# Kernel tuning notes

Hardware: AMD Instinct MI355X
Metric: run time of the kernel (lower is better)

The kernel has to match this reference:

```python
import jax, jax.numpy as jnp
import numpy as np

N = 50000
HEADS = 8
NEG_SLOPE = 0.2


def gat_layer(x, W, a_src, a_dst, b, src, dst, heads, n):
    # x: [N, Fin], W: [Fin, heads*C], a_src/a_dst: [heads, C], b: [heads*C]
    C = W.shape[1] // heads
    h = (x @ W).reshape(n, heads, C)                      # [N, H, C]
    al_s = jnp.einsum('nhc,hc->nh', h, a_src)             # [N, H]
    al_d = jnp.einsum('nhc,hc->nh', h, a_dst)             # [N, H]
    e = al_s[src] + al_d[dst]                             # [E, H]
    e = jnp.where(e > 0, e, NEG_SLOPE * e)                # LeakyReLU(0.2)
    # segment softmax over incoming edges of each destination node
    emax = jax.ops.segment_max(e, dst, num_segments=n)
    ex = jnp.exp(e - emax[dst])
    denom = jax.ops.segment_sum(ex, dst, num_segments=n)
    alpha = ex / denom[dst]                               # [E, H]
    out = jax.ops.segment_sum(h[src] * alpha[:, :, None], dst, num_segments=n)
    return out.reshape(n, heads * C) + b


def setup_inputs() -> dict:
    key = jax.random.key(0)
    ks = jax.random.split(key, 32)
    d_in, d_h, d_out = 128, 128, 128
    C = d_h // HEADS
    E = 800000
    x = jax.random.normal(ks[0], (N, d_in), dtype=jnp.float32)
    edge_index = jax.random.randint(ks[1], (2, E), 0, N, dtype=jnp.int64)
    edge_attr = jax.random.normal(ks[2], (E, 16), dtype=jnp.float32)
    s = lambda fan: 1.0 / np.sqrt(fan)
    inp = {'x': x, 'edge_index': edge_index, 'edge_attr': edge_attr}
    ki = 3
    for i in range(1, 5):
        fin = d_in if i == 1 else d_h
        inp[f'W{i}'] = jax.random.normal(ks[ki], (fin, d_h), jnp.float32) * s(fin); ki += 1
        inp[f'a_src{i}'] = jax.random.normal(ks[ki], (HEADS, C), jnp.float32) * s(C); ki += 1
        inp[f'a_dst{i}'] = jax.random.normal(ks[ki], (HEADS, C), jnp.float32) * s(C); ki += 1
        inp[f'b{i}'] = jnp.zeros((d_h,), jnp.float32)
    # conv5: heads=1, out=hidden
    inp['W5'] = jax.random.normal(ks[ki], (d_h, d_h), jnp.float32) * s(d_h); ki += 1
    inp['a_src5'] = jax.random.normal(ks[ki], (1, d_h), jnp.float32) * s(d_h); ki += 1
    inp['a_dst5'] = jax.random.normal(ks[ki], (1, d_h), jnp.float32) * s(d_h); ki += 1
    inp['b5'] = jnp.zeros((d_h,), jnp.float32)
    inp['W_lin'] = jax.random.normal(ks[ki], (d_h, d_out), jnp.float32) * s(d_h); ki += 1
    inp['b_lin'] = jnp.zeros((d_out,), jnp.float32)
    return inp


def reference(x, edge_index, edge_attr,
              W1, a_src1, a_dst1, b1,
              W2, a_src2, a_dst2, b2,
              W3, a_src3, a_dst3, b3,
              W4, a_src4, a_dst4, b4,
              W5, a_src5, a_dst5, b5,
              W_lin, b_lin):
    n = x.shape[0]
    # PyG GATConv adds self loops by default
    ar = jnp.arange(n, dtype=edge_index.dtype)
    src = jnp.concatenate([edge_index[0], ar])
    dst = jnp.concatenate([edge_index[1], ar])
    h = jax.nn.relu(gat_layer(x, W1, a_src1, a_dst1, b1, src, dst, HEADS, n))
    h = jax.nn.relu(gat_layer(h, W2, a_src2, a_dst2, b2, src, dst, HEADS, n))
    h = jax.nn.relu(gat_layer(h, W3, a_src3, a_dst3, b3, src, dst, HEADS, n))
    h = jax.nn.relu(gat_layer(h, W4, a_src4, a_dst4, b4, src, dst, HEADS, n))
    h = jax.nn.relu(gat_layer(h, W5, a_src5, a_dst5, b5, src, dst, 1, n))
    return jax.nn.relu(h @ W_lin + b_lin)
```

## Files before the change

### kernel.cpp

```cpp
#include <hip/hip_runtime.h>


typedef short short8 __attribute__((ext_vector_type(8)));
typedef float floatx4 __attribute__((ext_vector_type(4)));

__device__ __forceinline__ unsigned short f2bf(float f) {
  unsigned u = __float_as_uint(f);
  return (unsigned short)((u + 0x7FFF + ((u >> 16) & 1)) >> 16);
}
__device__ __forceinline__ float bf2f(unsigned short h) {
  return __uint_as_float(((unsigned)h) << 16);
}

__global__ __launch_bounds__(256) void k_deg_init(int* deg, int n) {
  int i = blockIdx.x * 256 + threadIdx.x;
  if (i < n) deg[i] = 1;
}

__global__ __launch_bounds__(256) void k_count(const int* __restrict__ ei, int E, int* deg) {
  int i = blockIdx.x * 256 + threadIdx.x;
  if (i < E) atomicAdd(&deg[ei[E + i]], 1);
}

__device__ __forceinline__ int block_excl_scan(int v, int* tot) {
  __shared__ int wsum[4];
  int lane = threadIdx.x & 63, w = threadIdx.x >> 6;
  int x = v;
  #pragma unroll
  for (int off = 1; off < 64; off <<= 1) {
    int y = __shfl_up(x, off);
    if (lane >= off) x += y;
  }
  if (lane == 63) wsum[w] = x;
  __syncthreads();
  int wbase = 0;
  #pragma unroll
  for (int i = 0; i < 4; i++) wbase += (i < w) ? wsum[i] : 0;
  if (tot) *tot = wsum[0] + wsum[1] + wsum[2] + wsum[3];
  return wbase + x - v;
}

__global__ __launch_bounds__(256) void k_bsum(const int* __restrict__ deg, int* __restrict__ bsum, int n) {
  int i = blockIdx.x * 256 + threadIdx.x;
  int v = (i < n) ? deg[i] : 0;
  int tot;
  block_excl_scan(v, &tot);
  if (threadIdx.x == 0) bsum[blockIdx.x] = tot;
}

__global__ __launch_bounds__(256) void k_bscan(const int* __restrict__ bsum, int* __restrict__ boff, int nb) {
  int t = threadIdx.x;
  int v = (t < nb) ? bsum[t] : 0;
  int ex = block_excl_scan(v, nullptr);
  if (t < nb) boff[t] = ex;
}

__global__ __launch_bounds__(256) void k_rowptr(const int* __restrict__ deg,
                                                const int* __restrict__ boff,
                                                int* __restrict__ row_ptr,
                                                int* __restrict__ cursor, int n) {
  int i = blockIdx.x * 256 + threadIdx.x;
  int v = (i < n) ? deg[i] : 0;
  int ex = block_excl_scan(v, nullptr) + boff[blockIdx.x];
  if (i < n) { row_ptr[i] = ex; cursor[i] = ex; }
  if (i == n - 1) row_ptr[n] = ex + v;
}

__global__ __launch_bounds__(256) void k_fill(const int* __restrict__ ei, int E, int n,
                                              int* cursor, int* __restrict__ srcs) {
  int i = blockIdx.x * 256 + threadIdx.x;
  if (i >= E + n) return;
  int s, d;
  if (i < E) { s = ei[i]; d = ei[E + i]; }
  else       { s = i - E; d = s; }
  int slot = atomicAdd(&cursor[d], 1);
  srcs[slot] = s;
}

__global__ __launch_bounds__(256) void k_cvt(const float* __restrict__ x,
                                             unsigned short* __restrict__ hi,
                                             unsigned short* __restrict__ lo, int n4) {
  int i = blockIdx.x * 256 + threadIdx.x;
  if (i >= n4) return;
  float4 v = ((const float4*)x)[i];
  ushort4 h, l;
  h.x = f2bf(v.x); l.x = f2bf(v.x - bf2f(h.x));
  h.y = f2bf(v.y); l.y = f2bf(v.y - bf2f(h.y));
  h.z = f2bf(v.z); l.z = f2bf(v.z - bf2f(h.z));
  h.w = f2bf(v.w); l.w = f2bf(v.w - bf2f(h.w));
  ((ushort4*)hi)[i] = h;
  ((ushort4*)lo)[i] = l;
}

__global__ __launch_bounds__(256) void k_cvt_w(const float* __restrict__ W,
                                               const float* __restrict__ a_s,
                                               const float* __restrict__ a_d,
                                               unsigned short* __restrict__ hi2,
                                               unsigned short* __restrict__ lo2, int H) {
  int b = blockIdx.x;
  if (b < 64) {
    int i = b * 256 + threadIdx.x;
    int k = i >> 7, n = i & 127;
    float v = W[i];
    unsigned short hh = f2bf(v), ll = f2bf(v - bf2f(hh));
    int nt = n >> 4, lr = n & 15;
    int j = k >> 5, kb = (k >> 3) & 3, e = k & 7;
    int off = ((j * 9 + nt) * 64 + kb * 16 + lr) * 8 + e;
    hi2[off] = hh; lo2[off] = ll;
    return;
  }
  if (H <= 0) return;
  int w = (b - 64) * 4 + (threadIdx.x >> 6);
  int lane = threadIdx.x & 63;
  int c0 = lane * 2;
  float2 wv = *(const float2*)(W + w * 128 + c0);
  float2 as2 = *(const float2*)(a_s + c0);
  float2 ad2 = *(const float2*)(a_d + c0);
  float ps = wv.x * as2.x + wv.y * as2.y;
  float pd = wv.x * ad2.x + wv.y * ad2.y;
  int C = 128 / H;
  int CL = C >> 1;
  for (int off = 1; off < CL; off <<= 1) {
    ps += __shfl_xor(ps, off);
    pd += __shfl_xor(pd, off);
  }
  if ((lane & (CL - 1)) == 0) {
    int hh = lane / CL;
    int j = w >> 5, kb = (w >> 3) & 3, e = w & 7;
    int base = ((j * 9 + 8) * 64 + kb * 16) * 8 + e;
    unsigned short hsv = f2bf(ps), lsv = f2bf(ps - bf2f(hsv));
    unsigned short hdv = f2bf(pd), ldv = f2bf(pd - bf2f(hdv));
    hi2[base + hh * 8] = hsv;       lo2[base + hh * 8] = lsv;
    hi2[base + (H + hh) * 8] = hdv; lo2[base + (H + hh) * 8] = ldv;
  }
}

__global__ __launch_bounds__(256) void k_gemm_bf(const unsigned short* __restrict__ Ahi,
                                                 const unsigned short* __restrict__ Alo,
                                                 const unsigned short* __restrict__ hi2,
                                                 const unsigned short* __restrict__ lo2,
                                                 const float* __restrict__ bias,
                                                 float* __restrict__ C,
                                                 float* __restrict__ als,
                                                 float* __restrict__ ald,
                                                 int M, int H, int relu) {
  int tid = threadIdx.x;
  int lane = tid & 63;
  int wv = tid >> 6;
  int m0 = blockIdx.x * 64 + wv * 16;
  int lr = lane & 15;
  int kb = lane >> 4;
  int arow = m0 + lr; if (arow >= M) arow = M - 1;
  const size_t abase = (size_t)arow * 128;

  short8 ahi[4], alo[4];
  #pragma unroll
  for (int j = 0; j < 4; j++) {
    int k0 = j * 32 + kb * 8;
    ahi[j] = *(const short8*)(Ahi + abase + k0);
    alo[j] = *(const short8*)(Alo + abase + k0);
  }

  floatx4 acc[9];
  #pragma unroll
  for (int nt = 0; nt < 9; nt++) acc[nt] = (floatx4){0.f, 0.f, 0.f, 0.f};

  #pragma unroll
  for (int j = 0; j < 4; j++) {
    #pragma unroll
    for (int nt = 0; nt < 9; nt++) {
      int boff = ((j * 9 + nt) * 64 + lane) * 8;
      short8 bhi = *(const short8*)(hi2 + boff);
      short8 blo = *(const short8*)(lo2 + boff);
      acc[nt] = __builtin_amdgcn_mfma_f32_16x16x32_bf16(ahi[j], bhi, acc[nt], 0, 0, 0);
      acc[nt] = __builtin_amdgcn_mfma_f32_16x16x32_bf16(ahi[j], blo, acc[nt], 0, 0, 0);
      acc[nt] = __builtin_amdgcn_mfma_f32_16x16x32_bf16(alo[j], bhi, acc[nt], 0, 0, 0);
    }
  }

  #pragma unroll
  for (int nt = 0; nt < 8; nt++) {
    int col = nt * 16 + lr;
    #pragma unroll
    for (int r = 0; r < 4; r++) {
      int row = m0 + kb * 4 + r;
      if (row < M) {
        float v = acc[nt][r];
        if (bias) v += bias[col];
        if (relu) v = fmaxf(v, 0.f);
        C[(size_t)row * 128 + col] = v;
      }
    }
  }
  if (als) {
    #pragma unroll
    for (int r = 0; r < 4; r++) {
      int row = m0 + kb * 4 + r;
      if (row < M) {
        float v = acc[8][r];
        if (H == 8) {
          if (lr < 8) als[row * 8 + lr] = v;
          else        ald[row * 8 + (lr - 8)] = v;
        } else {
          if (lr == 0) als[row] = v;
          else if (lr == 1) ald[row] = v;
        }
      }
    }
  }
}

template <int H>
__global__ __launch_bounds__(256) void k_agg(const int* __restrict__ row_ptr,
                                             const int* __restrict__ srcs,
                                             const float* __restrict__ als,
                                             const float* __restrict__ ald,
                                             const float* __restrict__ h,
                                             const float* __restrict__ bias,
                                             unsigned short* __restrict__ outHi,
                                             unsigned short* __restrict__ outLo, int n) {
  __shared__ float eL[4][128 * H];
  __shared__ int svL[4][128];
  const int EPP = 64 / H;
  int lane = threadIdx.x & 63;
  int wv = threadIdx.x >> 6;
  int v = blockIdx.x * 4 + wv;
  bool active = (v < n);
  int s0 = 0, s1 = 0;
  int eo = lane / H;
  int hd = lane % H;
  float ed = 0.f;
  if (active) { s0 = row_ptr[v]; s1 = row_ptr[v + 1]; ed = ald[v * H + hd]; }
  float m = -1e30f, d = 0.f;
  for (int j = s0 + eo; j < s1; j += EPP) {
    int sv = srcs[j];
    float e = als[sv * H + hd] + ed;
    e = (e > 0.f) ? e : 0.2f * e;
    int idx = j - s0;
    if (idx < 128) {
      eL[wv][idx * H + hd] = e;
      if (hd == 0) svL[wv][idx] = sv;
    }
    float nm = fmaxf(m, e);
    d = d * __expf(m - nm) + __expf(e - nm);
    m = nm;
  }
  #pragma unroll
  for (int off = H; off < 64; off <<= 1) {
    float om = __shfl_xor(m, off);
    float od = __shfl_xor(d, off);
    float nm = fmaxf(m, om);
    d = d * __expf(m - nm) + od * __expf(om - nm);
    m = nm;
  }
  float inv = 1.f / d;
  int nE = min(s1 - s0, 128);
  for (int t = lane; t < nE * H; t += 64)
    eL[wv][t] = __expf(eL[wv][t] - m) * inv;
  int c = lane * 2;
  int hd2 = (H == 8) ? (lane >> 3) : 0;
  float m2 = __shfl(m, hd2), inv2 = __shfl(inv, hd2), ed2 = __shfl(ed, hd2);
  float a0 = 0.f, a1 = 0.f;
  for (int jj = 0; jj < nE; ++jj) {
    int sv = svL[wv][jj];
    float al = eL[wv][jj * H + hd2];
    float2 hv = *(const float2*)(h + (size_t)sv * 128 + c);
    a0 += al * hv.x; a1 += al * hv.y;
  }
  for (int j = s0 + 128; j < s1; ++j) {
    int sv = srcs[j];
    float e = als[sv * H + hd2] + ed2;
    e = (e > 0.f) ? e : 0.2f * e;
    float al = __expf(e - m2) * inv2;
    float2 hv = *(const float2*)(h + (size_t)sv * 128 + c);
    a0 += al * hv.x; a1 += al * hv.y;
  }
  if (active) {
    a0 = fmaxf(a0 + bias[c], 0.f);
    a1 = fmaxf(a1 + bias[c + 1], 0.f);
    ushort2 h2, l2;
    h2.x = f2bf(a0); l2.x = f2bf(a0 - bf2f(h2.x));
    h2.y = f2bf(a1); l2.y = f2bf(a1 - bf2f(h2.y));
    *(ushort2*)(outHi + (size_t)v * 128 + c) = h2;
    *(ushort2*)(outLo + (size_t)v * 128 + c) = l2;
  }
}

extern "C" void kernel_launch(void* const* d_in, const int* in_sizes, int n_in,
                              void* d_out, int out_size, void* d_ws, size_t ws_size,
                              hipStream_t stream) {
  const float* x  = (const float*)d_in[0];
  const int*   ei = (const int*)d_in[1];
  const int N  = in_sizes[0] / 128;
  const int E  = in_sizes[1] / 2;
  const int ET = E + N;
  const int NB = (N + 255) / 256;

  const float *Wl[5], *as[5], *ad[5], *bl[5];
  for (int l = 0; l < 5; l++) {
    Wl[l] = (const float*)d_in[3 + 4 * l];
    as[l] = (const float*)d_in[4 + 4 * l];
    ad[l] = (const float*)d_in[5 + 4 * l];
    bl[l] = (const float*)d_in[6 + 4 * l];
  }
  const float* W_lin = (const float*)d_in[23];
  const float* b_lin = (const float*)d_in[24];

  char* p = (char*)d_ws;
  auto alloc = [&](size_t bytes) { void* r = (void*)p; p += (bytes + 255) & ~size_t(255); return r; };
  float* h    = (float*)alloc((size_t)N * 128 * 4);
  unsigned short* pAhi = (unsigned short*)alloc((size_t)N * 128 * 2);
  unsigned short* pAlo = (unsigned short*)alloc((size_t)N * 128 * 2);
  unsigned short* pBhi = (unsigned short*)alloc((size_t)N * 128 * 2);
  unsigned short* pBlo = (unsigned short*)alloc((size_t)N * 128 * 2);
  unsigned short* WtHi = (unsigned short*)alloc(144 * 128 * 2);
  unsigned short* WtLo = (unsigned short*)alloc(144 * 128 * 2);
  float* als  = (float*)alloc((size_t)N * 8 * 4);
  float* ald  = (float*)alloc((size_t)N * 8 * 4);
  int* row_ptr = (int*)alloc((size_t)(N + 1) * 4);
  int* cursor  = (int*)alloc((size_t)N * 4);
  int* deg     = (int*)alloc((size_t)N * 4);
  int* srcs    = (int*)alloc((size_t)ET * 4);
  int* bsum    = (int*)alloc((size_t)NB * 4);
  int* boff    = (int*)alloc((size_t)NB * 4);
  (void)ws_size; (void)n_in; (void)out_size;

  dim3 b256(256);
  k_deg_init<<<NB, b256, 0, stream>>>(deg, N);
  k_count<<<(E + 255) / 256, b256, 0, stream>>>(ei, E, deg);
  k_bsum<<<NB, b256, 0, stream>>>(deg, bsum, N);
  k_bscan<<<1, b256, 0, stream>>>(bsum, boff, NB);
  k_rowptr<<<NB, b256, 0, stream>>>(deg, boff, row_ptr, cursor, N);
  k_fill<<<(ET + 255) / 256, b256, 0, stream>>>(ei, E, N, cursor, srcs);

  int n4 = N * 128 / 4;
  k_cvt<<<(n4 + 255) / 256, b256, 0, stream>>>(x, pAhi, pAlo, n4);

  int gemm_grid = (N + 63) / 64;
  unsigned short *inHi = pAhi, *inLo = pAlo, *outHi = pBhi, *outLo = pBlo;
  for (int l = 0; l < 5; l++) {
    int H = (l < 4) ? 8 : 1;
    k_cvt_w<<<96, b256, 0, stream>>>(Wl[l], as[l], ad[l], WtHi, WtLo, H);
    k_gemm_bf<<<gemm_grid, b256, 0, stream>>>(inHi, inLo, WtHi, WtLo, nullptr,
                                              h, als, ald, N, H, 0);
    if (l < 4)
      k_agg<8><<<(N + 3) / 4, b256, 0, stream>>>(row_ptr, srcs, als, ald, h, bl[l], outHi, outLo, N);
    else
      k_agg<1><<<(N + 3) / 4, b256, 0, stream>>>(row_ptr, srcs, als, ald, h, bl[l], outHi, outLo, N);
    unsigned short* t;
    t = inHi; inHi = outHi; outHi = t;
    t = inLo; inLo = outLo; outLo = t;
  }
  k_cvt_w<<<96, b256, 0, stream>>>(W_lin, nullptr, nullptr, WtHi, WtLo, 0);
  k_gemm_bf<<<gemm_grid, b256, 0, stream>>>(inHi, inLo, WtHi, WtLo, b_lin,
                                            (float*)d_out, nullptr, nullptr, N, 0, 1);
}
```

Baseline: 717.9 us.

## Stage GEMM weight tiles in LDS and split aggregation across two edge slots

The GEMM kernel now copies the split-bf16 weight fragments into shared memory in two phases, so that waves read them from LDS and no longer each read them from global memory. The aggregation kernel now has each half-wave handle alternate edges with float4 loads over 4 channels, unrolled by two, and combines the halves with a cross-lane shuffle before writing the output. The goal is fewer, wider gather requests and more independent loads in flight per wave. In exchange the GEMM adds block barriers and 36 KB of LDS per block, which may lower occupancy.

```diff
diff --git a/kernel.cpp b/kernel.cpp
--- a/kernel.cpp
+++ b/kernel.cpp
@@ -144,6 +144,8 @@
                                                  float* __restrict__ als,
                                                  float* __restrict__ ald,
                                                  int M, int H, int relu) {
+  __shared__ unsigned short lHi[9216];
+  __shared__ unsigned short lLo[9216];
   int tid = threadIdx.x;
   int lane = tid & 63;
   int wv = tid >> 6;
@@ -166,15 +168,25 @@
   for (int nt = 0; nt < 9; nt++) acc[nt] = (floatx4){0.f, 0.f, 0.f, 0.f};
 
   #pragma unroll
-  for (int j = 0; j < 4; j++) {
+  for (int p = 0; p < 2; p++) {
+    if (p) __syncthreads();
+    for (int ci = tid; ci < 1152; ci += 256) {
+      ((short8*)lHi)[ci] = ((const short8*)(hi2 + p * 9216))[ci];
+      ((short8*)lLo)[ci] = ((const short8*)(lo2 + p * 9216))[ci];
+    }
+    __syncthreads();
     #pragma unroll
-    for (int nt = 0; nt < 9; nt++) {
-      int boff = ((j * 9 + nt) * 64 + lane) * 8;
-      short8 bhi = *(const short8*)(hi2 + boff);
-      short8 blo = *(const short8*)(lo2 + boff);
-      acc[nt] = __builtin_amdgcn_mfma_f32_16x16x32_bf16(ahi[j], bhi, acc[nt], 0, 0, 0);
-      acc[nt] = __builtin_amdgcn_mfma_f32_16x16x32_bf16(ahi[j], blo, acc[nt], 0, 0, 0);
-      acc[nt] = __builtin_amdgcn_mfma_f32_16x16x32_bf16(alo[j], bhi, acc[nt], 0, 0, 0);
+    for (int jj = 0; jj < 2; jj++) {
+      int j = p * 2 + jj;
+      #pragma unroll
+      for (int nt = 0; nt < 9; nt++) {
+        int boff = ((jj * 9 + nt) * 64 + lane) * 8;
+        short8 bhi = *(const short8*)(lHi + boff);
+        short8 blo = *(const short8*)(lLo + boff);
+        acc[nt] = __builtin_amdgcn_mfma_f32_16x16x32_bf16(ahi[j], bhi, acc[nt], 0, 0, 0);
+        acc[nt] = __builtin_amdgcn_mfma_f32_16x16x32_bf16(ahi[j], blo, acc[nt], 0, 0, 0);
+        acc[nt] = __builtin_amdgcn_mfma_f32_16x16x32_bf16(alo[j], bhi, acc[nt], 0, 0, 0);
+      }
     }
   }
 
@@ -257,32 +269,54 @@
   int nE = min(s1 - s0, 128);
   for (int t = lane; t < nE * H; t += 64)
     eL[wv][t] = __expf(eL[wv][t] - m) * inv;
-  int c = lane * 2;
-  int hd2 = (H == 8) ? (lane >> 3) : 0;
+  int slot = lane >> 5;
+  int l5 = lane & 31;
+  int c0 = l5 * 4;
+  int hd2 = (H == 8) ? (l5 >> 2) : 0;
   float m2 = __shfl(m, hd2), inv2 = __shfl(inv, hd2), ed2 = __shfl(ed, hd2);
-  float a0 = 0.f, a1 = 0.f;
-  for (int jj = 0; jj < nE; ++jj) {
-    int sv = svL[wv][jj];
-    float al = eL[wv][jj * H + hd2];
-    float2 hv = *(const float2*)(h + (size_t)sv * 128 + c);
-    a0 += al * hv.x; a1 += al * hv.y;
-  }
-  for (int j = s0 + 128; j < s1; ++j) {
+  float ax = 0.f, ay = 0.f, az = 0.f, aw = 0.f;
+  int jj = slot;
+  for (; jj + 2 < nE; jj += 4) {
+    int sv0 = svL[wv][jj], sv1 = svL[wv][jj + 2];
+    float al0 = eL[wv][jj * H + hd2], al1 = eL[wv][(jj + 2) * H + hd2];
+    float4 h0 = *(const float4*)(h + (size_t)sv0 * 128 + c0);
+    float4 h1 = *(const float4*)(h + (size_t)sv1 * 128 + c0);
+    ax += al0 * h0.x + al1 * h1.x;
+    ay += al0 * h0.y + al1 * h1.y;
+    az += al0 * h0.z + al1 * h1.z;
+    aw += al0 * h0.w + al1 * h1.w;
+  }
+  for (; jj < nE; jj += 2) {
+    int sv0 = svL[wv][jj];
+    float al0 = eL[wv][jj * H + hd2];
+    float4 h0 = *(const float4*)(h + (size_t)sv0 * 128 + c0);
+    ax += al0 * h0.x; ay += al0 * h0.y; az += al0 * h0.z; aw += al0 * h0.w;
+  }
+  for (int j = s0 + 128 + slot; j < s1; j += 2) {
     int sv = srcs[j];
     float e = als[sv * H + hd2] + ed2;
     e = (e > 0.f) ? e : 0.2f * e;
     float al = __expf(e - m2) * inv2;
-    float2 hv = *(const float2*)(h + (size_t)sv * 128 + c);
-    a0 += al * hv.x; a1 += al * hv.y;
-  }
-  if (active) {
-    a0 = fmaxf(a0 + bias[c], 0.f);
-    a1 = fmaxf(a1 + bias[c + 1], 0.f);
-    ushort2 h2, l2;
-    h2.x = f2bf(a0); l2.x = f2bf(a0 - bf2f(h2.x));
-    h2.y = f2bf(a1); l2.y = f2bf(a1 - bf2f(h2.y));
-    *(ushort2*)(outHi + (size_t)v * 128 + c) = h2;
-    *(ushort2*)(outLo + (size_t)v * 128 + c) = l2;
+    float4 hv = *(const float4*)(h + (size_t)sv * 128 + c0);
+    ax += al * hv.x; ay += al * hv.y; az += al * hv.z; aw += al * hv.w;
+  }
+  ax += __shfl_xor(ax, 32);
+  ay += __shfl_xor(ay, 32);
+  az += __shfl_xor(az, 32);
+  aw += __shfl_xor(aw, 32);
+  if (active && slot == 0) {
+    float o[4];
+    o[0] = fmaxf(ax + bias[c0 + 0], 0.f);
+    o[1] = fmaxf(ay + bias[c0 + 1], 0.f);
+    o[2] = fmaxf(az + bias[c0 + 2], 0.f);
+    o[3] = fmaxf(aw + bias[c0 + 3], 0.f);
+    ushort4 h4, l4;
+    h4.x = f2bf(o[0]); l4.x = f2bf(o[0] - bf2f(h4.x));
+    h4.y = f2bf(o[1]); l4.y = f2bf(o[1] - bf2f(h4.y));
+    h4.z = f2bf(o[2]); l4.z = f2bf(o[2] - bf2f(h4.z));
+    h4.w = f2bf(o[3]); l4.w = f2bf(o[3] - bf2f(h4.w));
+    *(ushort4*)(outHi + (size_t)v * 128 + c0) = h4;
+    *(ushort4*)(outLo + (size_t)v * 128 + c0) = l4;
   }
 }
 
```

After: 699.1 us. 1.03x faster.
